# Performance work log

Hardware: AMD Instinct MI355X
Metric: run time of the kernel (lower is better)

Reference implementation:

```python
import jax, jax.numpy as jnp
import numpy as np

NUM_CLASSES = 80
MAX_DET = 100
IOU_THR = 0.5
IMG = 2048.0
N_POINTS = 262144


def setup_inputs() -> dict:
    key = jax.random.key(0)
    k1, k2, k3, k4, k5 = jax.random.split(key, 5)
    class_preds = jax.random.normal(k1, (1, N_POINTS, NUM_CLASSES), jnp.float32)
    box_preds = jax.random.normal(k2, (1, N_POINTS, 4), jnp.float32)
    centerness_preds = jax.random.normal(k3, (1, N_POINTS, 1), jnp.float32)
    points = jax.random.uniform(k4, (N_POINTS, 2), jnp.float32) * IMG
    # per-point FPN strides in {8,16,32,64,128}
    lvl = jax.random.randint(k5, (N_POINTS, 1), 0, 5).astype(jnp.float32)
    strides = 8.0 * (2.0 ** lvl)
    return {"class_preds": class_preds, "box_preds": box_preds,
            "centerness_preds": centerness_preds, "points": points,
            "strides": strides}


def box_decode(enc, pts):
    # enc = (l, t, r, b) distances from point; pts = (px, py)
    px, py = pts[..., 0], pts[..., 1]
    l, t, r, b = enc[..., 0], enc[..., 1], enc[..., 2], enc[..., 3]
    return jnp.stack([px - l, py - t, px + r, py + b], axis=-1)


def pairwise_iou(a, b):
    area_a = (a[:, 2] - a[:, 0]) * (a[:, 3] - a[:, 1])
    area_b = (b[:, 2] - b[:, 0]) * (b[:, 3] - b[:, 1])
    lt = jnp.maximum(a[:, None, :2], b[None, :, :2])
    rb = jnp.minimum(a[:, None, 2:], b[None, :, 2:])
    wh = jnp.clip(rb - lt, 0.0)
    inter = wh[..., 0] * wh[..., 1]
    return inter / (area_a[:, None] + area_b[None, :] - inter + 1e-9)


def nms_fixed(boxes, scores, iou_thr):
    # Greedy NMS over a fixed, small candidate set. Returns score-sorted
    # order and a keep mask (static shapes; suppressed entries masked).
    K = boxes.shape[0]
    order = jnp.argsort(-scores)
    b = boxes[order]
    ious = pairwise_iou(b, b)  # [K, K]
    idx = jnp.arange(K)

    def body(i, keep):
        sup = (ious[i] > iou_thr) & (idx > i) & keep[i]
        return keep & ~sup

    keep = jax.lax.fori_loop(0, K, body, jnp.ones((K,), bool))
    return order, keep


def reference(class_preds, box_preds, centerness_preds, points, strides):
    B, N, C = class_preds.shape  # B == 1 (predict path assumes single image)
    # sqrt(sigmoid(cls) * sigmoid(centerness)), flattened over (point, class)
    scores = jnp.sqrt(jax.nn.sigmoid(class_preds) * jax.nn.sigmoid(centerness_preds))
    flat = scores.reshape(B, N * C)  # [1, N*C]
    _, top_idx = jax.lax.top_k(flat, MAX_DET)  # [1, K]
    pt_idx = top_idx // C                      # point index   [1, K]
    classes = top_idx % C                      # class index   [1, K]
    # NOTE: faithful to the original torch code, which gathers the flat score
    # tensor at the *point* index (indices), not at top_indices.
    sel_scores = flat[0, pt_idx[0]]            # [K]
    sel_boxes = box_preds[0, pt_idx[0]]        # [K, 4] (l,t,r,b)
    sel_points = points[pt_idx[0]]             # [K, 2]
    sel_strides = strides[pt_idx[0]]           # [K, 1]
    dec_boxes = box_decode(sel_boxes * sel_strides, sel_points)  # [K, 4]
    order, keep = nms_fixed(dec_boxes, sel_scores, IOU_THR)
    out_boxes = jnp.where(keep[:, None], dec_boxes[order], 0.0)
    out_scores = jnp.where(keep, sel_scores[order], 0.0)
    out_classes = jnp.where(keep, classes[0][order], -1)
    return out_boxes, out_scores, out_classes
```

## Files before the change

kernel.cpp:

```cpp
#include <hip/hip_runtime.h>


#define NPTS 262144
#define NCLS 80
#define NFLAT (NPTS * NCLS)
#define NF4 (NFLAT / 4)
#define KDET 100
#define HB 1024
#define HIST_LO 0.80f
#define HIST_SCALE 5120.0f
#define BINW (1.0f / HIST_SCALE)
#define THETA0 0.90f
#define MCAP 512
#define SBUF 512
#define NB1 1024
#define NT1 256

__device__ __forceinline__ float sigm(float x) {
    return __builtin_amdgcn_rcpf(1.0f + __expf(-x));
}

__global__ __launch_bounds__(NT1) void k_score_hist(
    const float* __restrict__ cls, const float* __restrict__ cent,
    unsigned* __restrict__ hist, unsigned* __restrict__ hdr,
    float* __restrict__ cscore, unsigned* __restrict__ cidx, int cap)
{
    __shared__ unsigned sh[HB];
    __shared__ float    sbs[SBUF];
    __shared__ unsigned sbi[SBUF];
    __shared__ unsigned sbn, sbase, sbm;
    __shared__ int      lastblk;
    for (int i = threadIdx.x; i < HB; i += NT1) sh[i] = 0;
    if (threadIdx.x == 0) sbn = 0;
    __syncthreads();

    const float4* c4 = (const float4*)cls;
    int tid = blockIdx.x * NT1 + threadIdx.x;
    #pragma unroll 2
    for (int it = 0; it < NF4 / (NB1 * NT1); ++it) {
        int g = tid + it * (NB1 * NT1);
        float4 v = c4[g];
        int p = g / 20;
        float sct = sigm(cent[p]);
        float sv[4] = {v.x, v.y, v.z, v.w};
        #pragma unroll
        for (int i = 0; i < 4; ++i) {
            float s = sqrtf(sigm(sv[i]) * sct);
            if (s >= HIST_LO) {
                int b = (int)((s - HIST_LO) * HIST_SCALE);
                if (b > HB - 1) b = HB - 1;
                atomicAdd(&sh[b], 1u);
                if (s >= THETA0) {
                    unsigned pos = atomicAdd(&sbn, 1u);
                    if (pos < SBUF) { sbs[pos] = s; sbi[pos] = (unsigned)(g * 4 + i); }
                    else {
                        unsigned q = atomicAdd(&hdr[0], 1u);
                        if (q < (unsigned)cap) { cscore[q] = s; cidx[q] = (unsigned)(g * 4 + i); }
                    }
                }
            }
        }
    }
    __syncthreads();
    for (int i = threadIdx.x; i < HB; i += NT1) {
        unsigned c = sh[i];
        if (c) atomicAdd(&hist[i], c);
    }
    if (threadIdx.x == 0) {
        unsigned m = sbn < SBUF ? sbn : SBUF;
        sbm = m;
        sbase = m ? atomicAdd(&hdr[0], m) : 0u;
    }
    __syncthreads();
    for (unsigned i = threadIdx.x; i < sbm; i += NT1) {
        unsigned q = sbase + i;
        if (q < (unsigned)cap) { cscore[q] = sbs[i]; cidx[q] = sbi[i]; }
    }
    __syncthreads();
    if (threadIdx.x == 0) {
        __threadfence();
        lastblk = (atomicAdd(&hdr[3], 1u) == NB1 - 1);
    }
    __syncthreads();
    if (!lastblk) return;
    __threadfence();
    for (int i = threadIdx.x; i < HB; i += NT1)
        sh[i] = __hip_atomic_load(&hist[i], __ATOMIC_RELAXED, __HIP_MEMORY_SCOPE_AGENT);
    __syncthreads();
    if (threadIdx.x == 0) {
        unsigned cum = 0; int T = -1;
        for (int b = HB - 1; b >= 0; --b) { cum += sh[b]; if (cum >= KDET) { T = b; break; } }
        unsigned cand = __hip_atomic_load(&hdr[0], __ATOMIC_RELAXED, __HIP_MEMORY_SCOPE_AGENT);
        int rescan;
        if (T < 0) { T = 0; rescan = 1; }
        else {
            float edge = HIST_LO + (float)T * BINW;
            rescan = (edge < THETA0 + 2.0f * BINW) || (cand > (unsigned)cap);
        }
        ((int*)hdr)[2] = T;
        if (rescan) hdr[0] = 0;
        __threadfence();
        hdr[1] = (unsigned)rescan;
    }
}

__global__ __launch_bounds__(NT1) void k_rescan(
    const float* __restrict__ cls, const float* __restrict__ cent,
    unsigned* __restrict__ hdr, float* __restrict__ cscore,
    unsigned* __restrict__ cidx, int cap)
{
    if (hdr[1] == 0) return;
    int T = ((int*)hdr)[2];
    const float4* c4 = (const float4*)cls;
    int tid = blockIdx.x * NT1 + threadIdx.x;
    #pragma unroll 1
    for (int it = 0; it < NF4 / (NB1 * NT1); ++it) {
        int g = tid + it * (NB1 * NT1);
        float4 v = c4[g];
        int p = g / 20;
        float sct = sigm(cent[p]);
        float sv[4] = {v.x, v.y, v.z, v.w};
        #pragma unroll
        for (int i = 0; i < 4; ++i) {
            float s = sqrtf(sigm(sv[i]) * sct);
            if (s >= HIST_LO) {
                int b = (int)((s - HIST_LO) * HIST_SCALE);
                if (b > HB - 1) b = HB - 1;
                if (b >= T) {
                    unsigned pos = atomicAdd(&hdr[0], 1u);
                    if (pos < (unsigned)cap) { cscore[pos] = s; cidx[pos] = (unsigned)(g * 4 + i); }
                }
            }
        }
    }
}

__global__ __launch_bounds__(256) void k_finalize(
    const float* __restrict__ cls, const float* __restrict__ cent,
    const float* __restrict__ boxp, const float* __restrict__ pts,
    const float* __restrict__ strd,
    const unsigned* __restrict__ hdr, const float* __restrict__ cscore,
    const unsigned* __restrict__ cidx, int cap, float* __restrict__ out)
{
    __shared__ float ss[MCAP];
    __shared__ unsigned si[MCAP];
    __shared__ unsigned mcnt;
    __shared__ float ioum[KDET * KDET];
    __shared__ float sel_s[KDET];
    __shared__ int   sel_c[KDET];
    __shared__ float sel_b[KDET][4];
    __shared__ int   ordv[KDET];
    __shared__ unsigned char keepA[KDET];
    __shared__ float bs[KDET][4];
    __shared__ float sso[KDET];
    __shared__ int   cso[KDET];

    int T = ((const int*)hdr)[2];
    unsigned n = hdr[0]; if (n > (unsigned)cap) n = (unsigned)cap;
    if (threadIdx.x == 0) mcnt = 0;
    __syncthreads();

    for (unsigned i = threadIdx.x; i < n; i += 256) {
        float s = cscore[i];
        int b = (int)((s - HIST_LO) * HIST_SCALE);
        if (b > HB - 1) b = HB - 1;
        if (b >= T) {
            unsigned p = atomicAdd(&mcnt, 1u);
            if (p < MCAP) { ss[p] = s; si[p] = cidx[i]; }
        }
    }
    __syncthreads();
    unsigned M = mcnt < MCAP ? mcnt : MCAP;
    for (unsigned i = threadIdx.x; i < MCAP; i += 256)
        if (i >= M) { ss[i] = -1.0f; si[i] = 0xFFFFFFFFu; }
    __syncthreads();

    for (int k2 = 2; k2 <= MCAP; k2 <<= 1) {
        for (int j = k2 >> 1; j > 0; j >>= 1) {
            for (int t = threadIdx.x; t < MCAP; t += 256) {
                int x = t ^ j;
                if (x > t) {
                    float s1 = ss[t], s2 = ss[x];
                    unsigned i1 = si[t], i2 = si[x];
                    bool rank21 = (s2 > s1) || (s2 == s1 && i2 < i1);
                    bool rank12 = (s1 > s2) || (s1 == s2 && i1 < i2);
                    bool doSwap = ((t & k2) == 0) ? rank21 : rank12;
                    if (doSwap) { ss[t] = s2; ss[x] = s1; si[t] = i2; si[x] = i1; }
                }
            }
            __syncthreads();
        }
    }

    if (threadIdx.x < KDET) {
        int k = threadIdx.x;
        unsigned j = si[k];
        if (ss[k] < 0.0f) j = 0;
        unsigned pt = j / (unsigned)NCLS;
        sel_c[k] = (int)(j % (unsigned)NCLS);
        sel_s[k] = sqrtf(sigm(cls[pt]) * sigm(cent[pt / (unsigned)NCLS]));
        float l = boxp[pt * 4 + 0], tt = boxp[pt * 4 + 1];
        float r = boxp[pt * 4 + 2], bb = boxp[pt * 4 + 3];
        float st = strd[pt];
        float px = pts[pt * 2 + 0], py = pts[pt * 2 + 1];
        sel_b[k][0] = __fsub_rn(px, __fmul_rn(l,  st));
        sel_b[k][1] = __fsub_rn(py, __fmul_rn(tt, st));
        sel_b[k][2] = __fadd_rn(px, __fmul_rn(r,  st));
        sel_b[k][3] = __fadd_rn(py, __fmul_rn(bb, st));
    }
    __syncthreads();

    if (threadIdx.x < KDET) {
        int k = threadIdx.x; float sk = sel_s[k]; int rank = 0;
        for (int j = 0; j < KDET; ++j) {
            float sj = sel_s[j];
            if (sj > sk || (sj == sk && j < k)) ++rank;
        }
        ordv[rank] = k;
    }
    __syncthreads();
    if (threadIdx.x < KDET) {
        int i = threadIdx.x, o = ordv[i];
        sso[i] = sel_s[o]; cso[i] = sel_c[o];
        bs[i][0] = sel_b[o][0]; bs[i][1] = sel_b[o][1];
        bs[i][2] = sel_b[o][2]; bs[i][3] = sel_b[o][3];
        keepA[i] = 1;
    }
    __syncthreads();

    for (int t = threadIdx.x; t < KDET * KDET; t += 256) {
        int i = t / KDET, j = t % KDET;
        float ax1 = bs[i][0], ay1 = bs[i][1], ax2 = bs[i][2], ay2 = bs[i][3];
        float bx1 = bs[j][0], by1 = bs[j][1], bx2 = bs[j][2], by2 = bs[j][3];
        float areaA = (ax2 - ax1) * (ay2 - ay1);
        float areaB = (bx2 - bx1) * (by2 - by1);
        float lx = fmaxf(ax1, bx1), ly = fmaxf(ay1, by1);
        float rx = fminf(ax2, bx2), ry = fminf(ay2, by2);
        float w = fmaxf(rx - lx, 0.0f), h = fmaxf(ry - ly, 0.0f);
        float inter = w * h;
        ioum[t] = inter / (areaA + areaB - inter + 1e-9f);
    }
    __syncthreads();

    for (int i = 0; i < KDET; ++i) {
        if (keepA[i]) {
            int j = threadIdx.x;
            if (j > i && j < KDET && ioum[i * KDET + j] > 0.5f) keepA[j] = 0;
        }
        __syncthreads();
    }

    if (threadIdx.x < KDET) {
        int i = threadIdx.x;
        bool kp = keepA[i] != 0;
        out[i * 4 + 0] = kp ? bs[i][0] : 0.0f;
        out[i * 4 + 1] = kp ? bs[i][1] : 0.0f;
        out[i * 4 + 2] = kp ? bs[i][2] : 0.0f;
        out[i * 4 + 3] = kp ? bs[i][3] : 0.0f;
        out[4 * KDET + i] = kp ? sso[i] : 0.0f;
        out[5 * KDET + i] = kp ? (float)cso[i] : -1.0f;
    }
}

extern "C" void kernel_launch(void* const* d_in, const int* in_sizes, int n_in,
                              void* d_out, int out_size, void* d_ws, size_t ws_size,
                              hipStream_t stream)
{
    const float* cls  = (const float*)d_in[0];
    const float* boxp = (const float*)d_in[1];
    const float* cent = (const float*)d_in[2];
    const float* pts  = (const float*)d_in[3];
    const float* strd = (const float*)d_in[4];
    float* out = (float*)d_out;

    char* ws = (char*)d_ws;
    unsigned* hdr  = (unsigned*)ws;
    unsigned* hist = (unsigned*)(ws + 16);
    size_t capS = ws_size > 4360 ? (ws_size - 4352) / 8 : 64;
    int cap = (int)(capS > 32768 ? 32768 : capS);
    float*    cscore = (float*)(ws + 4352);
    unsigned* cidx   = (unsigned*)(ws + 4352 + (size_t)cap * 4);

    hipMemsetAsync(d_ws, 0, 4112, stream);
    hipLaunchKernelGGL(k_score_hist, dim3(NB1), dim3(NT1), 0, stream,
                       cls, cent, hist, hdr, cscore, cidx, cap);
    hipLaunchKernelGGL(k_rescan, dim3(NB1), dim3(NT1), 0, stream,
                       cls, cent, hdr, cscore, cidx, cap);
    hipLaunchKernelGGL(k_finalize, dim3(1), dim3(256), 0, stream,
                       cls, cent, boxp, pts, strd, hdr, cscore, cidx, cap, out);
}
```

Before: 249.1 us.

## Fully unroll score pass, threshold in reciprocal domain, replace sort with rank-select

The first pass now launches enough blocks that each thread handles exactly 8 float4s. All loads are issued up front to raise memory-level parallelism. Thresholding compares the product of (1+exp) terms against precomputed reciprocal bounds, so sqrt and rcp only run for candidates. The candidate threshold rises to 0.94 with a one-bin safety margin. In finalize, candidates are rescored with precise sigmoid and the top-100 are picked by O(M^2) rank counting instead of a bitonic sort, and NMS runs in a single wavefront using shuffles instead of 100 block barriers. The raised threshold risks more rescans, and the precise rescoring could change tie ordering.

```diff
diff --git a/kernel.cpp b/kernel.cpp
--- a/kernel.cpp
+++ b/kernel.cpp
@@ -10,14 +10,25 @@
 #define HIST_LO 0.80f
 #define HIST_SCALE 5120.0f
 #define BINW (1.0f / HIST_SCALE)
-#define THETA0 0.90f
-#define MCAP 512
+#define THETA0 0.94f
+#define W_CAND (1.0f / (THETA0 * THETA0))
+#define W_HIST (1.0f / (HIST_LO * HIST_LO))
+#define MCAP 1024
 #define SBUF 512
-#define NB1 1024
+#define NB1 2560
 #define NT1 256
-
-__device__ __forceinline__ float sigm(float x) {
-    return __builtin_amdgcn_rcpf(1.0f + __expf(-x));
+#define UB 8
+#define TT (NB1 * NT1)
+
+__device__ __forceinline__ float s_from_w(float w) {
+    return sqrtf(__builtin_amdgcn_rcpf(w));
+}
+__device__ __forceinline__ float sigm_p(float x) {
+    return 1.0f / (1.0f + expf(-x));
+}
+__device__ __forceinline__ int bin_of(float s) {
+    int b = (int)((s - HIST_LO) * HIST_SCALE);
+    return b < 0 ? 0 : (b > HB - 1 ? HB - 1 : b);
 }
 
 __global__ __launch_bounds__(NT1) void k_score_hist(
@@ -36,21 +47,26 @@
 
     const float4* c4 = (const float4*)cls;
     int tid = blockIdx.x * NT1 + threadIdx.x;
-    #pragma unroll 2
-    for (int it = 0; it < NF4 / (NB1 * NT1); ++it) {
-        int g = tid + it * (NB1 * NT1);
-        float4 v = c4[g];
-        int p = g / 20;
-        float sct = sigm(cent[p]);
-        float sv[4] = {v.x, v.y, v.z, v.w};
+
+    float4 v[UB];
+    float  cb[UB];
+    #pragma unroll
+    for (int u = 0; u < UB; ++u) v[u] = c4[tid + u * TT];
+    #pragma unroll
+    for (int u = 0; u < UB; ++u) cb[u] = cent[(tid + u * TT) / 20];
+
+    #pragma unroll
+    for (int u = 0; u < UB; ++u) {
+        int g = tid + u * TT;
+        float f = 1.0f + __expf(-cb[u]);
+        float sv[4] = {v[u].x, v[u].y, v[u].z, v[u].w};
         #pragma unroll
         for (int i = 0; i < 4; ++i) {
-            float s = sqrtf(sigm(sv[i]) * sct);
-            if (s >= HIST_LO) {
-                int b = (int)((s - HIST_LO) * HIST_SCALE);
-                if (b > HB - 1) b = HB - 1;
-                atomicAdd(&sh[b], 1u);
-                if (s >= THETA0) {
+            float w = (1.0f + __expf(-sv[i])) * f;
+            if (w <= W_HIST) {
+                float s = s_from_w(w);
+                atomicAdd(&sh[bin_of(s)], 1u);
+                if (w <= W_CAND) {
                     unsigned pos = atomicAdd(&sbn, 1u);
                     if (pos < SBUF) { sbs[pos] = s; sbi[pos] = (unsigned)(g * 4 + i); }
                     else {
@@ -79,7 +95,7 @@
     __syncthreads();
     if (threadIdx.x == 0) {
         __threadfence();
-        lastblk = (atomicAdd(&hdr[3], 1u) == NB1 - 1);
+        lastblk = (atomicAdd(&hdr[3], 1u) == (unsigned)(gridDim.x - 1));
     }
     __syncthreads();
     if (!lastblk) return;
@@ -94,8 +110,8 @@
         int rescan;
         if (T < 0) { T = 0; rescan = 1; }
         else {
-            float edge = HIST_LO + (float)T * BINW;
-            rescan = (edge < THETA0 + 2.0f * BINW) || (cand > (unsigned)cap);
+            float edgeTm1 = HIST_LO + (float)(T - 1) * BINW;
+            rescan = (edgeTm1 < THETA0 + 2.0f * BINW) || (cand > (unsigned)cap);
         }
         ((int*)hdr)[2] = T;
         if (rescan) hdr[0] = 0;
@@ -110,23 +126,27 @@
     unsigned* __restrict__ cidx, int cap)
 {
     if (hdr[1] == 0) return;
-    int T = ((int*)hdr)[2];
+    int T = ((const int*)hdr)[2];
+    int Tm = T > 0 ? T - 1 : 0;
     const float4* c4 = (const float4*)cls;
     int tid = blockIdx.x * NT1 + threadIdx.x;
-    #pragma unroll 1
-    for (int it = 0; it < NF4 / (NB1 * NT1); ++it) {
-        int g = tid + it * (NB1 * NT1);
-        float4 v = c4[g];
-        int p = g / 20;
-        float sct = sigm(cent[p]);
-        float sv[4] = {v.x, v.y, v.z, v.w};
+    float4 v[UB];
+    float  cb[UB];
+    #pragma unroll
+    for (int u = 0; u < UB; ++u) v[u] = c4[tid + u * TT];
+    #pragma unroll
+    for (int u = 0; u < UB; ++u) cb[u] = cent[(tid + u * TT) / 20];
+    #pragma unroll
+    for (int u = 0; u < UB; ++u) {
+        int g = tid + u * TT;
+        float f = 1.0f + __expf(-cb[u]);
+        float sv[4] = {v[u].x, v[u].y, v[u].z, v[u].w};
         #pragma unroll
         for (int i = 0; i < 4; ++i) {
-            float s = sqrtf(sigm(sv[i]) * sct);
-            if (s >= HIST_LO) {
-                int b = (int)((s - HIST_LO) * HIST_SCALE);
-                if (b > HB - 1) b = HB - 1;
-                if (b >= T) {
+            float w = (1.0f + __expf(-sv[i])) * f;
+            if (w <= W_HIST) {
+                float s = s_from_w(w);
+                if (bin_of(s) >= Tm) {
                     unsigned pos = atomicAdd(&hdr[0], 1u);
                     if (pos < (unsigned)cap) { cscore[pos] = s; cidx[pos] = (unsigned)(g * 4 + i); }
                 }
@@ -142,63 +162,62 @@
     const unsigned* __restrict__ hdr, const float* __restrict__ cscore,
     const unsigned* __restrict__ cidx, int cap, float* __restrict__ out)
 {
-    __shared__ float ss[MCAP];
+    __shared__ float    ss[MCAP];
     __shared__ unsigned si[MCAP];
+    __shared__ float    ps[MCAP];
     __shared__ unsigned mcnt;
-    __shared__ float ioum[KDET * KDET];
+    __shared__ float    tks[KDET];
+    __shared__ unsigned tkj[KDET];
     __shared__ float sel_s[KDET];
     __shared__ int   sel_c[KDET];
     __shared__ float sel_b[KDET][4];
     __shared__ int   ordv[KDET];
-    __shared__ unsigned char keepA[KDET];
     __shared__ float bs[KDET][4];
     __shared__ float sso[KDET];
     __shared__ int   cso[KDET];
+    __shared__ unsigned char keepA[KDET];
+    __shared__ float ioum[KDET * KDET];
 
     int T = ((const int*)hdr)[2];
+    int Tm = T > 0 ? T - 1 : 0;
     unsigned n = hdr[0]; if (n > (unsigned)cap) n = (unsigned)cap;
     if (threadIdx.x == 0) mcnt = 0;
     __syncthreads();
 
     for (unsigned i = threadIdx.x; i < n; i += 256) {
         float s = cscore[i];
-        int b = (int)((s - HIST_LO) * HIST_SCALE);
-        if (b > HB - 1) b = HB - 1;
-        if (b >= T) {
+        if (bin_of(s) >= Tm) {
             unsigned p = atomicAdd(&mcnt, 1u);
             if (p < MCAP) { ss[p] = s; si[p] = cidx[i]; }
         }
     }
     __syncthreads();
     unsigned M = mcnt < MCAP ? mcnt : MCAP;
-    for (unsigned i = threadIdx.x; i < MCAP; i += 256)
-        if (i >= M) { ss[i] = -1.0f; si[i] = 0xFFFFFFFFu; }
-    __syncthreads();
-
-    for (int k2 = 2; k2 <= MCAP; k2 <<= 1) {
-        for (int j = k2 >> 1; j > 0; j >>= 1) {
-            for (int t = threadIdx.x; t < MCAP; t += 256) {
-                int x = t ^ j;
-                if (x > t) {
-                    float s1 = ss[t], s2 = ss[x];
-                    unsigned i1 = si[t], i2 = si[x];
-                    bool rank21 = (s2 > s1) || (s2 == s1 && i2 < i1);
-                    bool rank12 = (s1 > s2) || (s1 == s2 && i1 < i2);
-                    bool doSwap = ((t & k2) == 0) ? rank21 : rank12;
-                    if (doSwap) { ss[t] = s2; ss[x] = s1; si[t] = i2; si[x] = i1; }
-                }
-            }
-            __syncthreads();
-        }
-    }
+
+    for (unsigned m = threadIdx.x; m < M; m += 256) {
+        unsigned j = si[m];
+        ps[m] = sqrtf(sigm_p(cls[j]) * sigm_p(cent[j / (unsigned)NCLS]));
+    }
+    if (threadIdx.x < KDET) { tks[threadIdx.x] = -1.0f; tkj[threadIdx.x] = 0u; }
+    __syncthreads();
+
+    for (unsigned m = threadIdx.x; m < M; m += 256) {
+        float sm = ps[m]; unsigned jm = si[m];
+        int rank = 0;
+        for (unsigned q = 0; q < M; ++q) {
+            float sq = ps[q]; unsigned jq = si[q];
+            if (sq > sm || (sq == sm && jq < jm)) ++rank;
+        }
+        if (rank < KDET) { tks[rank] = sm; tkj[rank] = jm; }
+    }
+    __syncthreads();
 
     if (threadIdx.x < KDET) {
         int k = threadIdx.x;
-        unsigned j = si[k];
-        if (ss[k] < 0.0f) j = 0;
+        unsigned j = tkj[k];
         unsigned pt = j / (unsigned)NCLS;
         sel_c[k] = (int)(j % (unsigned)NCLS);
-        sel_s[k] = sqrtf(sigm(cls[pt]) * sigm(cent[pt / (unsigned)NCLS]));
+        sel_s[k] = sqrtf(sigm_p(cls[pt]) * sigm_p(cent[pt / (unsigned)NCLS]));
         float l = boxp[pt * 4 + 0], tt = boxp[pt * 4 + 1];
         float r = boxp[pt * 4 + 2], bb = boxp[pt * 4 + 3];
         float st = strd[pt];
@@ -242,13 +261,24 @@
     }
     __syncthreads();
 
-    for (int i = 0; i < KDET; ++i) {
-        if (keepA[i]) {
-            int j = threadIdx.x;
-            if (j > i && j < KDET && ioum[i * KDET + j] > 0.5f) keepA[j] = 0;
-        }
-        __syncthreads();
-    }
+    if (threadIdx.x < 64) {
+        int L = threadIdx.x;
+        int k0 = 1, k1 = 1;
+        #pragma unroll 1
+        for (int i = 0; i < KDET; ++i) {
+            int owner = (i < 64) ? i : (i - 64);
+            int flag  = (i < 64) ? k0 : k1;
+            int keep_i = __shfl(flag, owner, 64);
+            if (keep_i) {
+                if (L > i && ioum[i * KDET + L] > 0.5f) k0 = 0;
+                int j2 = L + 64;
+                if (j2 > i && j2 < KDET && ioum[i * KDET + j2] > 0.5f) k1 = 0;
+            }
+        }
+        keepA[L] = (unsigned char)k0;
+        if (L + 64 < KDET) keepA[L + 64] = (unsigned char)k1;
+    }
+    __syncthreads();
 
     if (threadIdx.x < KDET) {
         int i = threadIdx.x;
```

Result: slower. 291.8 us (+17.1%).
